# Performance work log

Hardware: AMD Instinct MI355X
Metric: run time of the kernel (lower is better)

Reference implementation:

```python
import jax, jax.numpy as jnp
import numpy as np

CAPACITY = 0.5


def setup_inputs() -> dict:
    key = jax.random.key(0)
    ks = jax.random.split(key, 5)
    b, s, d, dff = 4, 4096, 1024, 4096
    x = jax.random.normal(ks[0], (b, s, d), dtype=jnp.float32)
    attention_mask = jnp.ones((b, s), dtype=jnp.int32)
    Wr = jax.random.normal(ks[1], (d, 1), dtype=jnp.float32) * (1.0 / np.sqrt(d))
    br = jnp.zeros((1,), dtype=jnp.float32)
    W1 = jax.random.normal(ks[2], (d, dff), dtype=jnp.float32) * (1.0 / np.sqrt(d))
    b1 = jnp.zeros((dff,), dtype=jnp.float32)
    W2 = jax.random.normal(ks[3], (dff, d), dtype=jnp.float32) * (1.0 / np.sqrt(dff))
    b2 = jnp.zeros((d,), dtype=jnp.float32)
    return {"x": x, "attention_mask": attention_mask, "Wr": Wr, "br": br,
            "W1": W1, "b1": b1, "W2": W2, "b2": b2}


def _block(filtered_x, router_weights, W1, b1, W2, b2):
    # Stand-in MoD block: residual router-weighted GELU MLP.
    h = jax.nn.gelu(jnp.einsum('bkd,df->bkf', filtered_x, W1) + b1)
    out = jnp.einsum('bkf,fd->bkd', h, W2) + b2
    return filtered_x + router_weights * out  # router_weights: [b,k,1]


def reference(x, attention_mask, Wr, br, W1, b1, W2, b2):
    b, s, d = x.shape
    top_k = int(s * CAPACITY)
    router_logits = jnp.einsum('bsd,do->bso', x, Wr) + br        # [b,s,1]
    scores = jax.nn.sigmoid(router_logits[..., 0])               # [b,s]
    token_weights, token_index = jax.lax.top_k(scores, top_k)    # [b,k]
    sort_order = jnp.argsort(token_index, axis=1)                # positions
    sorted_indices = jnp.take_along_axis(token_index, sort_order, axis=1)  # [b,k]
    filtered_x = jnp.take_along_axis(x, sorted_indices[..., None], axis=1)  # [b,k,d]
    tw = jax.nn.softmax(token_weights, axis=1)                   # softmax over k
    router_weights = jnp.take_along_axis(tw, sort_order, axis=1)[..., None]  # [b,k,1]
    block_out = _block(filtered_x, router_weights, W1, b1, W2, b2)
    batch_idx = jnp.arange(b)[:, None]
    hidden_states = x.at[batch_idx, sorted_indices].set(block_out)
    # aux loss: BCE-with-logits, targets = 1 on selected tokens
    targets = jnp.zeros((b, s), dtype=x.dtype).at[batch_idx, sorted_indices].set(1.0)
    l = router_logits[..., 0]
    aux_loss = jnp.mean(jnp.maximum(l, 0.0) - l * targets + jnp.log1p(jnp.exp(-jnp.abs(l))))
    return hidden_states, aux_loss
```

## Files before the change

kernel.cpp:

```cpp
#include <hip/hip_runtime.h>

#define NB 4
#define SEQ 4096
#define DIM 1024
#define DFF 4096
#define KSEL 2048
#define NTOK (NB * SEQ)
#define MR (NB * KSEL)

typedef float f32x4_t __attribute__((ext_vector_type(4)));
typedef unsigned long u64_t;
typedef unsigned long u64x2_t __attribute__((ext_vector_type(2)));
typedef int i32x8_t __attribute__((ext_vector_type(8)));

__device__ __forceinline__ unsigned char f2fp8(float f) {
  return (unsigned char)(__builtin_amdgcn_cvt_pk_fp8_f32(f, f, 0, false) & 0xff);
}

__device__ __forceinline__ int kperm(int kb) {
  return ((kb >> 3) & 3) * 32 + (kb >> 5) * 8 + (kb & 7);
}

#define GLD16(g, l) __builtin_amdgcn_global_load_lds( \
    (const __attribute__((address_space(1))) void*)(g), \
    (__attribute__((address_space(3))) void*)(l), 16, 0, 0)

__global__ void prep_kernel(const float* __restrict__ W1, unsigned char* __restrict__ W1t,
                            const float* __restrict__ W2, unsigned char* __restrict__ W2t,
                            const float* __restrict__ x, const float* __restrict__ Wr,
                            const float* __restrict__ br,
                            float* __restrict__ logits, float* __restrict__ scores) {
  __shared__ float tl[32][33];
  int bid = blockIdx.x;
  if (bid < 8192) {
    const float* W; unsigned char* Wt; int R, C, bx, by;
    if (bid < 4096) { W = W1; Wt = W1t; R = DIM; C = DFF; bx = bid & 127; by = bid >> 7; }
    else { bid -= 4096; W = W2; Wt = W2t; R = DFF; C = DIM; bx = bid & 31; by = bid >> 5; }
    int c0 = bx * 32;
    int r0 = by * 32;
    int tx = threadIdx.x & 31, ty = threadIdx.x >> 5;
#pragma unroll
    for (int i = 0; i < 4; ++i)
      tl[ty + i * 8][tx] = W[(size_t)(r0 + ty + i * 8) * C + c0 + tx];
    __syncthreads();
    int k = r0 + tx;
    int pos = (k & ~127) + kperm(k & 127);
#pragma unroll
    for (int i = 0; i < 4; ++i)
      Wt[(size_t)(c0 + ty + i * 8) * R + pos] = f2fp8(16.f * tl[tx][ty + i * 8]);
  } else {
    int lane = threadIdx.x & 63;
    int wid  = threadIdx.x >> 6;
    int row  = (bid - 8192) * 4 + wid;
    const float4* xr = (const float4*)(x + (size_t)row * DIM);
    const float4* w4 = (const float4*)Wr;
    float sum = 0.f;
#pragma unroll
    for (int i = 0; i < 4; ++i) {
      float4 a = xr[lane + i * 64];
      float4 w = w4[lane + i * 64];
      sum += a.x * w.x + a.y * w.y + a.z * w.z + a.w * w.w;
    }
#pragma unroll
    for (int off = 32; off > 0; off >>= 1) sum += __shfl_down(sum, off);
    if (lane == 0) {
      float l = sum + br[0];
      logits[row] = l;
      scores[row] = 1.f / (1.f + expf(-l));
    }
  }
}

__global__ void rank_kernel(const float* __restrict__ scores, int* __restrict__ sel) {
  __shared__ float s_sc[SEQ];
  int batch = blockIdx.x >> 8;
  int chunk = blockIdx.x & 255;
  int t = threadIdx.x;
  const float4* sb4 = (const float4*)(scores + batch * SEQ);
  float4* ls4 = (float4*)s_sc;
#pragma unroll
  for (int i = 0; i < 4; ++i) ls4[t + i * 256] = sb4[t + i * 256];
  __syncthreads();
  int tok = chunk * 16 + (t >> 4);
  int sg  = t & 15;
  float s = s_sc[tok];
  const float4* seg = ls4 + sg * 64;
  int jbase = sg * 256;
  int rank = 0;
#pragma unroll 4
  for (int j4 = 0; j4 < 64; ++j4) {
    float4 v = seg[j4];
    int j = jbase + j4 * 4;
    rank += (v.x > s || (v.x == s && j     < tok)) ? 1 : 0;
    rank += (v.y > s || (v.y == s && j + 1 < tok)) ? 1 : 0;
    rank += (v.z > s || (v.z == s && j + 2 < tok)) ? 1 : 0;
    rank += (v.w > s || (v.w == s && j + 3 < tok)) ? 1 : 0;
  }
#pragma unroll
  for (int off = 8; off > 0; off >>= 1) rank += __shfl_down(rank, off, 16);
  if (sg == 0) sel[batch * SEQ + tok] = (rank < KSEL) ? 1 : 0;
}

__global__ void pack_kernel(const float* __restrict__ scores, const int* __restrict__ sel,
                            int* __restrict__ rows, float* __restrict__ rwv,
                            int* __restrict__ slot) {
  __shared__ float red[16];
  __shared__ int scn[1024];
  int batch = blockIdx.x;
  int t = threadIdx.x;
  const float* sb = scores + batch * SEQ;
  const int* fb = sel + batch * SEQ;
  float sc[4]; int fl[4];
#pragma unroll
  for (int i = 0; i < 4; ++i) { sc[i] = sb[t * 4 + i]; fl[i] = fb[t * 4 + i]; }
  float m = fmaxf(fmaxf(sc[0], sc[1]), fmaxf(sc[2], sc[3]));
#pragma unroll
  for (int off = 32; off > 0; off >>= 1) m = fmaxf(m, __shfl_down(m, off));
  if ((t & 63) == 0) red[t >> 6] = m;
  __syncthreads();
  if (t == 0) { float v = red[0]; for (int i = 1; i < 16; ++i) v = fmaxf(v, red[i]); red[0] = v; }
  __syncthreads();
  m = red[0];
  __syncthreads();
  float ex[4]; float esum = 0.f;
#pragma unroll
  for (int i = 0; i < 4; ++i) { ex[i] = expf(sc[i] - m); if (fl[i]) esum += ex[i]; }
#pragma unroll
  for (int off = 32; off > 0; off >>= 1) esum += __shfl_down(esum, off);
  if ((t & 63) == 0) red[t >> 6] = esum;
  __syncthreads();
  if (t == 0) { float v = 0.f; for (int i = 0; i < 16; ++i) v += red[i]; red[0] = v; }
  __syncthreads();
  float total = red[0];
  int cnt = fl[0] + fl[1] + fl[2] + fl[3];
  scn[t] = cnt;
  __syncthreads();
  for (int off = 1; off < 1024; off <<= 1) {
    int a = scn[t];
    int b = (t >= off) ? scn[t - off] : 0;
    __syncthreads();
    scn[t] = a + b;
    __syncthreads();
  }
  int p = scn[t] - cnt;
#pragma unroll
  for (int i = 0; i < 4; ++i) {
    if (fl[i]) {
      rows[batch * KSEL + p] = t * 4 + i;
      rwv[batch * KSEL + p]  = ex[i] / total;
      slot[batch * SEQ + t * 4 + i] = batch * KSEL + p;
      ++p;
    }
  }
}

__global__ void gather_copy_kernel(const float* __restrict__ x, const int* __restrict__ sel,
                                   const int* __restrict__ slot,
                                   unsigned char* __restrict__ Xc, float* __restrict__ out) {
  int tokg = blockIdx.x;
  const float4* src = (const float4*)(x + (size_t)tokg * DIM);
  int t = threadIdx.x;
  float4 v = src[t];
  if (sel[tokg]) {
    unsigned lo = (unsigned)__builtin_amdgcn_cvt_pk_fp8_f32(v.x, v.y, 0, false);
    unsigned both = (unsigned)__builtin_amdgcn_cvt_pk_fp8_f32(v.z, v.w, (int)lo, true);
    int mrow = slot[tokg];
    int panel = mrow >> 7, rowp = mrow & 127;
    int k = t * 4;
    int pos = kperm(k & 127);
    size_t addr = (size_t)panel * (128 * DIM) + (size_t)(k >> 7) * 16384
                + (size_t)(pos >> 5) * 4096 + (size_t)rowp * 32 + (pos & 31);
    *(unsigned*)(Xc + addr) = both;
  } else {
    ((float4*)(out + (size_t)tokg * DIM))[t] = v;
  }
}

template <int EPI>
__global__ __launch_bounds__(256)
void gemm14(const unsigned char* __restrict__ A, const unsigned char* __restrict__ Bt,
            int M, int N, int K,
            const float* __restrict__ bias,
            unsigned char* __restrict__ Hout,
            const float* __restrict__ x,
            const int* __restrict__ rows,
            const float* __restrict__ rwv,
            float* __restrict__ out) {
  __shared__ __align__(16) unsigned char Bs[128 * 128];

  const int t = threadIdx.x;
  const int lane = t & 63;
  const int wid = t >> 6;
  const int wm = wid >> 1;
  const int wn = wid & 1;

  const int nwg = gridDim.x;
  const int qq = nwg >> 3;
  const int nid = (blockIdx.x & 7) * qq + (blockIdx.x >> 3);
  const int gx = N / 128;
  const int by = nid / gx;
  const int bx = nid - by * gx;
  const int bm0 = by * 128;
  const int bn0 = bx * 128;

  const size_t ldb = (size_t)K;
  const char* Bb = (const char*)Bt + (size_t)bn0 * ldb;
  char* BsB = (char*)Bs;

  const int srow = t >> 3;
  const size_t stage_off = (size_t)srow * ldb + (size_t)((((t & 7) ^ (srow & 7)) * 16));

  const int cbs0 = ((lane >> 4) * 32     ) ^ ((lane & 7) << 4);
  const int cbs1 = ((lane >> 4) * 32 + 16) ^ ((lane & 7) << 4);

  const char* Ap = (const char*)A + (size_t)by * 128 * (size_t)K + (size_t)(lane >> 4) * 4096;
  const char* arow[4];
#pragma unroll
  for (int i = 0; i < 4; ++i)
    arow[i] = Ap + (size_t)(wm * 64 + i * 16 + (lane & 15)) * 32;

  f32x4_t acc[4][4];
  f32x4_t zero = {0.f, 0.f, 0.f, 0.f};
#pragma unroll
  for (int i = 0; i < 4; ++i)
#pragma unroll
    for (int j = 0; j < 4; ++j) acc[i][j] = zero;

  const int NT = K / 128;

  for (int kt = 0; kt < NT; ++kt) {
    i32x8_t am[4];
#pragma unroll
    for (int i = 0; i < 4; ++i)
      am[i] = *(const i32x8_t*)(arow[i] + (size_t)kt * 16384);
    const size_t kb = (size_t)kt * 128 + stage_off;
#pragma unroll
    for (int c = 0; c < 4; ++c)
      GLD16(Bb + kb + (size_t)(c * 32) * ldb, BsB + t * 16 + c * 4096);
    __syncthreads();

    i32x8_t bq[4];
#pragma unroll
    for (int j = 0; j < 4; ++j) {
      const char* bp = BsB + (wn * 64 + j * 16 + (lane & 15)) * 128;
      union { u64x2_t q[2]; i32x8_t v; } u;
      u.q[0] = *(const u64x2_t*)(bp + cbs0);
      u.q[1] = *(const u64x2_t*)(bp + cbs1);
      bq[j] = u.v;
    }
    __builtin_amdgcn_s_setprio(1);
#pragma unroll
    for (int i = 0; i < 4; ++i)
#pragma unroll
      for (int j = 0; j < 4; ++j)
        acc[i][j] = __builtin_amdgcn_mfma_scale_f32_16x16x128_f8f6f4(
            am[i], bq[j], acc[i][j], 0, 0,
            0, 0x7f7f7f7f, 0, 0x7f7f7f7f);
    __builtin_amdgcn_s_setprio(0);
    __syncthreads();
  }

  const int rb = (lane >> 4) * 4;
  const int cc = lane & 15;
#pragma unroll
  for (int i = 0; i < 4; ++i) {
#pragma unroll
    for (int qi = 0; qi < 4; ++qi) {
      int grow = bm0 + wm * 64 + i * 16 + rb + qi;
      if (EPI == 1) {
        int panel = grow >> 7, rowp = grow & 127;
#pragma unroll
        for (int j = 0; j < 4; ++j) {
          int gcol = bn0 + wn * 64 + j * 16 + cc;
          float v = acc[i][j][qi] * 0.0625f + bias[gcol];
          float cp = 0.7978845608028654f * (v + 0.044715f * v * v * v);
          float g = v / (1.f + __expf(-2.f * cp));
          int pos = kperm(gcol & 127);
          size_t addr = (size_t)panel * (128 * DFF) + (size_t)(gcol >> 7) * 16384
                      + (size_t)(pos >> 5) * 4096 + (size_t)rowp * 32 + (pos & 31);
          Hout[addr] = f2fp8(g);
        }
      } else {
        int batch = grow >> 11;
        int tok = rows[grow];
        float rw = rwv[grow];
        size_t obase = ((size_t)(batch * SEQ + tok)) * DIM;
#pragma unroll
        for (int j = 0; j < 4; ++j) {
          int gcol = bn0 + wn * 64 + j * 16 + cc;
          float v = acc[i][j][qi] * 0.0625f + bias[gcol];
          out[obase + gcol] = x[obase + gcol] + rw * v;
        }
      }
    }
  }
}

__global__ void aux_kernel(const float* __restrict__ logits, const int* __restrict__ sel,
                           float* __restrict__ out, int out_size) {
  __shared__ float red[16];
  int t = threadIdx.x;
  float sum = 0.f;
  for (int i = t; i < NTOK; i += 1024) {
    float l = logits[i];
    float tgt = sel[i] ? 1.f : 0.f;
    sum += fmaxf(l, 0.f) - l * tgt + log1pf(expf(-fabsf(l)));
  }
#pragma unroll
  for (int off = 32; off > 0; off >>= 1) sum += __shfl_down(sum, off);
  if ((t & 63) == 0) red[t >> 6] = sum;
  __syncthreads();
  if (t == 0) {
    float v = 0.f;
    for (int i = 0; i < 16; ++i) v += red[i];
    out[out_size - 1] = v / (float)NTOK;
  }
}

extern "C" void kernel_launch(void* const* d_in, const int* in_sizes, int n_in,
                              void* d_out, int out_size, void* d_ws, size_t ws_size,
                              hipStream_t stream) {
  const float* x  = (const float*)d_in[0];
  const float* Wr = (const float*)d_in[2];
  const float* br = (const float*)d_in[3];
  const float* W1 = (const float*)d_in[4];
  const float* b1 = (const float*)d_in[5];
  const float* W2 = (const float*)d_in[6];
  const float* b2 = (const float*)d_in[7];
  float* out = (float*)d_out;

  char* ws = (char*)d_ws;
  float* logits = (float*)(ws);
  float* scores = (float*)(ws + 65536);
  int*   sel    = (int*)(ws + 131072);
  int*   rows   = (int*)(ws + 196608);
  float* rwv    = (float*)(ws + 229376);
  int*   slot   = (int*)(ws + 262144);
  unsigned char* W1t = (unsigned char*)(ws + 327680);
  unsigned char* W2t = (unsigned char*)(ws + 327680 + 4194304);
  unsigned char* Xc  = (unsigned char*)(ws + 327680 + 2 * 4194304);
  unsigned char* H   = (unsigned char*)(ws + 327680 + 2 * 4194304 + 8388608);

  prep_kernel<<<12288, 256, 0, stream>>>(W1, W1t, W2, W2t, x, Wr, br, logits, scores);
  rank_kernel<<<NTOK / 16, 256, 0, stream>>>(scores, sel);
  pack_kernel<<<NB, 1024, 0, stream>>>(scores, sel, rows, rwv, slot);
  gather_copy_kernel<<<NTOK, 256, 0, stream>>>(x, sel, slot, Xc, out);
  gemm14<1><<<(MR / 128) * (DFF / 128), 256, 0, stream>>>(
      Xc, W1t, MR, DFF, DIM, b1, H, nullptr, nullptr, nullptr, nullptr);
  gemm14<2><<<(MR / 128) * (DIM / 128), 256, 0, stream>>>(
      H, W2t, MR, DIM, DFF, b2, nullptr, x, rows, rwv, out);
  aux_kernel<<<1, 1024, 0, stream>>>(logits, sel, out, out_size);
}
```

Baseline: 203.0 us.

## Double-buffer GEMM B tiles and move the residual copy into the router pass

The GEMM main loop now keeps two LDS buffers for B and two register sets for A. The next k-tile is prefetched while the current one runs through MFMA, using vmcnt waits and raw barriers in place of a load-sync-compute-sync loop, so global-load latency can be hidden. The router pass in prep_kernel now also copies every x row into the output, which lets the gather kernel launch only over selected rows and drops the slot array. The cost is a full extra write of x, since selected rows are later overwritten, plus doubled LDS per workgroup, which may lower occupancy.

```diff
diff --git a/kernel.cpp b/kernel.cpp
--- a/kernel.cpp
+++ b/kernel.cpp
@@ -29,7 +29,8 @@
                             const float* __restrict__ W2, unsigned char* __restrict__ W2t,
                             const float* __restrict__ x, const float* __restrict__ Wr,
                             const float* __restrict__ br,
-                            float* __restrict__ logits, float* __restrict__ scores) {
+                            float* __restrict__ logits, float* __restrict__ scores,
+                            float* __restrict__ out) {
   __shared__ float tl[32][33];
   int bid = blockIdx.x;
   if (bid < 8192) {
@@ -53,12 +54,14 @@
     int wid  = threadIdx.x >> 6;
     int row  = (bid - 8192) * 4 + wid;
     const float4* xr = (const float4*)(x + (size_t)row * DIM);
+    float4* orow = (float4*)(out + (size_t)row * DIM);
     const float4* w4 = (const float4*)Wr;
     float sum = 0.f;
 #pragma unroll
     for (int i = 0; i < 4; ++i) {
       float4 a = xr[lane + i * 64];
       float4 w = w4[lane + i * 64];
+      orow[lane + i * 64] = a;
       sum += a.x * w.x + a.y * w.y + a.z * w.z + a.w * w.w;
     }
 #pragma unroll
@@ -102,8 +105,7 @@
 }
 
 __global__ void pack_kernel(const float* __restrict__ scores, const int* __restrict__ sel,
-                            int* __restrict__ rows, float* __restrict__ rwv,
-                            int* __restrict__ slot) {
+                            int* __restrict__ rows, float* __restrict__ rwv) {
   __shared__ float red[16];
   __shared__ int scn[1024];
   int batch = blockIdx.x;
@@ -148,37 +150,32 @@
     if (fl[i]) {
       rows[batch * KSEL + p] = t * 4 + i;
       rwv[batch * KSEL + p]  = ex[i] / total;
-      slot[batch * SEQ + t * 4 + i] = batch * KSEL + p;
       ++p;
     }
   }
 }
 
-__global__ void gather_copy_kernel(const float* __restrict__ x, const int* __restrict__ sel,
-                                   const int* __restrict__ slot,
-                                   unsigned char* __restrict__ Xc, float* __restrict__ out) {
-  int tokg = blockIdx.x;
-  const float4* src = (const float4*)(x + (size_t)tokg * DIM);
+__global__ void gather_kernel(const float* __restrict__ x, const int* __restrict__ rows,
+                              unsigned char* __restrict__ Xc) {
+  int mrow = blockIdx.x;
+  int batch = mrow >> 11;
+  int tok = rows[mrow];
+  const float4* src = (const float4*)(x + ((size_t)(batch * SEQ + tok)) * DIM);
   int t = threadIdx.x;
   float4 v = src[t];
-  if (sel[tokg]) {
-    unsigned lo = (unsigned)__builtin_amdgcn_cvt_pk_fp8_f32(v.x, v.y, 0, false);
-    unsigned both = (unsigned)__builtin_amdgcn_cvt_pk_fp8_f32(v.z, v.w, (int)lo, true);
-    int mrow = slot[tokg];
-    int panel = mrow >> 7, rowp = mrow & 127;
-    int k = t * 4;
-    int pos = kperm(k & 127);
-    size_t addr = (size_t)panel * (128 * DIM) + (size_t)(k >> 7) * 16384
-                + (size_t)(pos >> 5) * 4096 + (size_t)rowp * 32 + (pos & 31);
-    *(unsigned*)(Xc + addr) = both;
-  } else {
-    ((float4*)(out + (size_t)tokg * DIM))[t] = v;
-  }
+  unsigned lo = (unsigned)__builtin_amdgcn_cvt_pk_fp8_f32(v.x, v.y, 0, false);
+  unsigned both = (unsigned)__builtin_amdgcn_cvt_pk_fp8_f32(v.z, v.w, (int)lo, true);
+  int panel = mrow >> 7, rowp = mrow & 127;
+  int k = t * 4;
+  int pos = kperm(k & 127);
+  size_t addr = (size_t)panel * (128 * DIM) + (size_t)(k >> 7) * 16384
+              + (size_t)(pos >> 5) * 4096 + (size_t)rowp * 32 + (pos & 31);
+  *(unsigned*)(Xc + addr) = both;
 }
 
 template <int EPI>
 __global__ __launch_bounds__(256)
-void gemm14(const unsigned char* __restrict__ A, const unsigned char* __restrict__ Bt,
+void gemm15(const unsigned char* __restrict__ A, const unsigned char* __restrict__ Bt,
             int M, int N, int K,
             const float* __restrict__ bias,
             unsigned char* __restrict__ Hout,
@@ -186,7 +183,7 @@
             const int* __restrict__ rows,
             const float* __restrict__ rwv,
             float* __restrict__ out) {
-  __shared__ __align__(16) unsigned char Bs[128 * 128];
+  __shared__ __align__(16) unsigned char Bs[2][128 * 128];
 
   const int t = threadIdx.x;
   const int lane = t & 63;
@@ -205,7 +202,6 @@
 
   const size_t ldb = (size_t)K;
   const char* Bb = (const char*)Bt + (size_t)bn0 * ldb;
-  char* BsB = (char*)Bs;
 
   const int srow = t >> 3;
   const size_t stage_off = (size_t)srow * ldb + (size_t)((((t & 7) ^ (srow & 7)) * 16));
@@ -228,21 +224,25 @@
 
   const int NT = K / 128;
 
-  for (int kt = 0; kt < NT; ++kt) {
-    i32x8_t am[4];
+  i32x8_t amA[4], amB[4];
+
+  auto loadA = [&](i32x8_t* am, int kt) {
 #pragma unroll
     for (int i = 0; i < 4; ++i)
       am[i] = *(const i32x8_t*)(arow[i] + (size_t)kt * 16384);
+  };
+  auto stageB = [&](int buf, int kt) {
     const size_t kb = (size_t)kt * 128 + stage_off;
+    char* dst = (char*)Bs[buf] + t * 16;
 #pragma unroll
     for (int c = 0; c < 4; ++c)
-      GLD16(Bb + kb + (size_t)(c * 32) * ldb, BsB + t * 16 + c * 4096);
-    __syncthreads();
-
+      GLD16(Bb + kb + (size_t)(c * 32) * ldb, dst + c * 4096);
+  };
+  auto compute = [&](const i32x8_t* am, int buf) {
     i32x8_t bq[4];
 #pragma unroll
     for (int j = 0; j < 4; ++j) {
-      const char* bp = BsB + (wn * 64 + j * 16 + (lane & 15)) * 128;
+      const char* bp = (const char*)Bs[buf] + (wn * 64 + j * 16 + (lane & 15)) * 128;
       union { u64x2_t q[2]; i32x8_t v; } u;
       u.q[0] = *(const u64x2_t*)(bp + cbs0);
       u.q[1] = *(const u64x2_t*)(bp + cbs1);
@@ -257,7 +257,30 @@
             am[i], bq[j], acc[i][j], 0, 0,
             0, 0x7f7f7f7f, 0, 0x7f7f7f7f);
     __builtin_amdgcn_s_setprio(0);
-    __syncthreads();
+  };
+
+  loadA(amA, 0);
+  stageB(0, 0);
+
+  for (int kt = 0; kt < NT; kt += 2) {
+    loadA(amB, kt + 1);
+    stageB(1, kt + 1);
+    asm volatile("s_waitcnt vmcnt(8)" ::: "memory");
+    __builtin_amdgcn_s_barrier();
+    __builtin_amdgcn_sched_barrier(0);
+    compute(amA, 0);
+    __builtin_amdgcn_s_barrier();
+    if (kt + 2 < NT) {
+      loadA(amA, kt + 2);
+      stageB(0, kt + 2);
+      asm volatile("s_waitcnt vmcnt(8)" ::: "memory");
+    } else {
+      asm volatile("s_waitcnt vmcnt(0)" ::: "memory");
+    }
+    __builtin_amdgcn_s_barrier();
+    __builtin_amdgcn_sched_barrier(0);
+    compute(amB, 1);
+    __builtin_amdgcn_s_barrier();
   }
 
   const int rb = (lane >> 4) * 4;
@@ -335,19 +358,18 @@
   int*   sel    = (int*)(ws + 131072);
   int*   rows   = (int*)(ws + 196608);
   float* rwv    = (float*)(ws + 229376);
-  int*   slot   = (int*)(ws + 262144);
   unsigned char* W1t = (unsigned char*)(ws + 327680);
   unsigned char* W2t = (unsigned char*)(ws + 327680 + 4194304);
   unsigned char* Xc  = (unsigned char*)(ws + 327680 + 2 * 4194304);
   unsigned char* H   = (unsigned char*)(ws + 327680 + 2 * 4194304 + 8388608);
 
-  prep_kernel<<<12288, 256, 0, stream>>>(W1, W1t, W2, W2t, x, Wr, br, logits, scores);
+  prep_kernel<<<12288, 256, 0, stream>>>(W1, W1t, W2, W2t, x, Wr, br, logits, scores, out);
   rank_kernel<<<NTOK / 16, 256, 0, stream>>>(scores, sel);
-  pack_kernel<<<NB, 1024, 0, stream>>>(scores, sel, rows, rwv, slot);
-  gather_copy_kernel<<<NTOK, 256, 0, stream>>>(x, sel, slot, Xc, out);
-  gemm14<1><<<(MR / 128) * (DFF / 128), 256, 0, stream>>>(
+  pack_kernel<<<NB, 1024, 0, stream>>>(scores, sel, rows, rwv);
+  gather_kernel<<<MR, 256, 0, stream>>>(x, rows, Xc);
+  gemm15<1><<<(MR / 128) * (DFF / 128), 256, 0, stream>>>(
       Xc, W1t, MR, DFF, DIM, b1, H, nullptr, nullptr, nullptr, nullptr);
-  gemm14<2><<<(MR / 128) * (DIM / 128), 256, 0, stream>>>(
+  gemm15<2><<<(MR / 128) * (DIM / 128), 256, 0, stream>>>(
       H, W2t, MR, DIM, DFF, b2, nullptr, x, rows, rwv, out);
   aux_kernel<<<1, 1024, 0, stream>>>(logits, sel, out, out_size);
 }
```

Result: no change. 200.8 us (-1.1%).
